# Performance work log

Hardware: AMD Instinct MI355X
Metric: run time of the kernel (lower is better)

## Reference

```python
import jax, jax.numpy as jnp
import numpy as np

B, S = 32, 4096
HID, MEM, ATT = 512, 512, 512


def setup_inputs() -> dict:
    key = jax.random.key(0)
    k1, k2, k3, k4, k5, k6, k7 = jax.random.split(key, 7)
    scale_h = 1.0 / np.sqrt(HID)
    scale_m = 1.0 / np.sqrt(MEM)
    scale_a = 1.0 / np.sqrt(ATT)
    return {
        "hidden": jax.random.normal(k1, (B, HID), dtype=jnp.float32),
        "memory": jax.random.normal(k2, (B, S, MEM), dtype=jnp.float32),
        "mem_pad": jnp.zeros((B, S), dtype=jnp.bool_),
        "coverage": jax.random.uniform(k3, (B, S), dtype=jnp.float32),
        # params stored as (in, out) so x @ W == torch Linear(x)
        "W_h": jax.random.uniform(k4, (HID, ATT), minval=-scale_h, maxval=scale_h, dtype=jnp.float32),
        "W_m": jax.random.uniform(k5, (MEM, ATT), minval=-scale_m, maxval=scale_m, dtype=jnp.float32),
        "W_c": jax.random.uniform(k6, (ATT,), minval=-1.0, maxval=1.0, dtype=jnp.float32),
        "v": jax.random.uniform(k7, (ATT,), minval=-scale_a, maxval=scale_a, dtype=jnp.float32),
    }


def reference(hidden, memory, mem_pad, coverage, W_h, W_m, W_c, v):
    h = hidden @ W_h                                   # (B, A)
    m = jnp.einsum('bsd,da->bsa', memory, W_m)         # (B, S, A)
    c_feat = coverage[..., None] * W_c                 # (B, S, A) ; Linear(1->A) == scalar * weight row
    score = jnp.einsum('bsa,a->bs', jnp.tanh(h[:, None, :] + m + c_feat), v)  # (B, S)
    score = jnp.where(mem_pad, -jnp.inf, score)
    attn_weights = jax.nn.softmax(score, axis=-1)      # (B, S)
    context = jnp.einsum('bs,bsd->bd', attn_weights, memory)  # (B, D)
    return context, attn_weights
```

## Files before the change

kernel.cpp:

```cpp
#include <hip/hip_runtime.h>
#include <hip/hip_bf16.h>
#include <math.h>

#define BB 32
#define SS 4096
#define DMEM 512
#define DATT 512

typedef short short8 __attribute__((ext_vector_type(8)));
typedef float floatx4 __attribute__((ext_vector_type(4)));

__device__ inline short f2bf(float x) {
    unsigned u = __float_as_uint(x);
    unsigned r = (u + 0x7fffu + ((u >> 16) & 1u)) >> 16;
    return (short)(r & 0xffffu);
}

__device__ inline float fast_tanh(float x) {
    float e = __expf(2.0f * x);
    float r = __builtin_amdgcn_rcpf(e + 1.0f);
    return __builtin_fmaf(-2.0f, r, 1.0f);
}

__device__ inline void gld_lds16(const void* g, void* l) {
    __builtin_amdgcn_global_load_lds(
        (const __attribute__((address_space(1))) unsigned int*)g,
        (__attribute__((address_space(3))) unsigned int*)l, 16, 0, 0);
}


__global__ void prep_wt_kernel(const float* __restrict__ Wm, short* __restrict__ Wt) {
    const int n0 = blockIdx.x * 32;
    const int k0 = blockIdx.y * 32;
    const int t = threadIdx.x;
    const int r = t >> 5, c = t & 31;
    __shared__ float lds[32 * 33];
#pragma unroll
    for (int j = 0; j < 4; ++j) {
        int kk = r + j * 8;
        lds[kk * 33 + c] = Wm[(size_t)(k0 + kk) * 512 + n0 + c];
    }
    __syncthreads();
#pragma unroll
    for (int j = 0; j < 4; ++j) {
        int nn = r + j * 8;
        Wt[(size_t)(n0 + nn) * 512 + k0 + c] = f2bf(lds[c * 33 + nn]);
    }
}

__global__ void prep_h_kernel(const float* __restrict__ hidden, const float* __restrict__ Wh,
                              float* __restrict__ h) {
    const int b = blockIdx.x;
    const int n = blockIdx.y * 256 + threadIdx.x;
    const int kc = blockIdx.z;
    float acc = 0.f;
#pragma unroll 8
    for (int k = kc * 128; k < kc * 128 + 128; ++k)
        acc += hidden[b * 512 + k] * Wh[(size_t)k * 512 + n];
    atomicAdd(&h[b * 512 + n], acc);
}


__global__ __launch_bounds__(512, 2)
void fused_kernel(const float* __restrict__ memory,
                  const float* __restrict__ coverage,
                  const unsigned char* __restrict__ pad,
                  const short* __restrict__ Wt,
                  const float* __restrict__ h,
                  const float* __restrict__ Wc,
                  const float* __restrict__ v,
                  float* __restrict__ pOut,
                  float* __restrict__ mWS,
                  float* __restrict__ lWS,
                  float* __restrict__ ctxPart) {
    const int blk = blockIdx.x;
    const int b = blk >> 5;
    const int st = blk & 31;
    const int s0 = st * 128;

    const int tid = threadIdx.x;
    const int lane = tid & 63;
    const int wave = tid >> 6;
    const int wm = wave & 1;
    const int wn = wave >> 1;
    const int col = lane & 15;
    const int q = lane >> 4;

    __shared__ __align__(16) char smem[77824];
    char* tileB0 = smem;
    char* tileB1 = smem + 32768;
    char* tileA  = smem + 65536;
    float* covS   = (float*)(smem + 73728);
    float* sred   = (float*)(smem + 74240);
    float* scoreS = (float*)(smem + 76288);
    float* pS     = (float*)(smem + 76800);
    float* mlS    = (float*)(smem + 77312);
    float4* red4  = (float4*)smem;

    if (tid < 128) covS[tid] = coverage[(size_t)b * SS + s0 + tid];

    const float4* gA4 = (const float4*)(memory + ((size_t)b * SS + s0) * 512);
    const char* gB = (const char*)Wt;

    float4 apf[2];

    floatx4 acc[4][8];
#pragma unroll
    for (int mi = 0; mi < 4; ++mi)
#pragma unroll
        for (int ni = 0; ni < 8; ++ni)
            acc[mi][ni] = (floatx4){0.f, 0.f, 0.f, 0.f};

#pragma unroll
    for (int j = 0; j < 2; ++j) {
        int s = j * 512 + tid;
        apf[j] = gA4[(size_t)(s >> 3) * 128 + (s & 7)];
    }
#pragma unroll
    for (int it = 0; it < 4; ++it) {
        int ci = it * 512 + tid;
        int row = ci >> 2;
        int gch = (ci & 3) ^ ((row >> 1) & 3);
        gld_lds16(gB + (size_t)row * 1024 + gch * 16,
                  tileB0 + it * 8192 + wave * 1024);
    }
#pragma unroll
    for (int j = 0; j < 2; ++j) {
        int s = j * 512 + tid;
        int row = s >> 3, l8 = s & 7;
        union { __hip_bfloat162 h2; unsigned u; } p0, p1;
        p0.h2 = __float22bfloat162_rn(make_float2(apf[j].x, apf[j].y));
        p1.h2 = __float22bfloat162_rn(make_float2(apf[j].z, apf[j].w));
        uint2 w; w.x = p0.u; w.y = p1.u;
        int off = row * 64 + (((l8 >> 1) ^ ((row >> 1) & 3)) << 4) + ((l8 & 1) << 3);
        *(uint2*)(tileA + off) = w;
    }
    __syncthreads();

    for (int kt = 0; kt < 16; ++kt) {
        if (kt < 15) {
#pragma unroll
            for (int j = 0; j < 2; ++j) {
                int s = j * 512 + tid;
                apf[j] = gA4[(size_t)(s >> 3) * 128 + (kt + 1) * 8 + (s & 7)];
            }
            char* ldsB = ((kt + 1) & 1) ? tileB1 : tileB0;
#pragma unroll
            for (int it = 0; it < 4; ++it) {
                int ci = it * 512 + tid;
                int row = ci >> 2;
                int gch = (ci & 3) ^ ((row >> 1) & 3);
                gld_lds16(gB + (size_t)row * 1024 + (kt + 1) * 64 + gch * 16,
                          ldsB + it * 8192 + wave * 1024);
            }
        }

        const char* bbase = (kt & 1) ? tileB1 : tileB0;
        short8 af[4], bf[8];
#pragma unroll
        for (int mi = 0; mi < 4; ++mi) {
            int row = wm * 64 + mi * 16 + col;
            af[mi] = *(const short8*)(tileA + row * 64 + ((q ^ ((row >> 1) & 3)) << 4));
        }
#pragma unroll
        for (int ni = 0; ni < 8; ++ni) {
            int row = wn * 128 + ni * 16 + col;
            bf[ni] = *(const short8*)(bbase + row * 64 + ((q ^ ((row >> 1) & 3)) << 4));
        }
#pragma unroll
        for (int mi = 0; mi < 4; ++mi)
#pragma unroll
            for (int ni = 0; ni < 8; ++ni)
                acc[mi][ni] = __builtin_amdgcn_mfma_f32_16x16x32_bf16(af[mi], bf[ni], acc[mi][ni], 0, 0, 0);

        __syncthreads();

        if (kt < 15) {
#pragma unroll
            for (int j = 0; j < 2; ++j) {
                int s = j * 512 + tid;
                int row = s >> 3, l8 = s & 7;
                union { __hip_bfloat162 h2; unsigned u; } p0, p1;
                p0.h2 = __float22bfloat162_rn(make_float2(apf[j].x, apf[j].y));
                p1.h2 = __float22bfloat162_rn(make_float2(apf[j].z, apf[j].w));
                uint2 w; w.x = p0.u; w.y = p1.u;
                int off = row * 64 + (((l8 >> 1) ^ ((row >> 1) & 3)) << 4) + ((l8 & 1) << 3);
                *(uint2*)(tileA + off) = w;
            }
            __syncthreads();
        }
    }

    float hv[8], wcv[8], vv[8];
#pragma unroll
    for (int ni = 0; ni < 8; ++ni) {
        int n = wn * 128 + ni * 16 + col;
        hv[ni] = h[b * 512 + n];
        wcv[ni] = Wc[n];
        vv[ni] = v[n];
    }
    float rowAcc[4][4];
#pragma unroll
    for (int mi = 0; mi < 4; ++mi)
#pragma unroll
        for (int r = 0; r < 4; ++r)
            rowAcc[mi][r] = 0.f;
#pragma unroll
    for (int mi = 0; mi < 4; ++mi) {
#pragma unroll
        for (int r = 0; r < 4; ++r) {
            float cv = covS[wm * 64 + mi * 16 + q * 4 + r];
#pragma unroll
            for (int ni = 0; ni < 8; ++ni) {
                float val = acc[mi][ni][r] + hv[ni] + cv * wcv[ni];
                rowAcc[mi][r] += fast_tanh(val) * vv[ni];
            }
        }
    }
#pragma unroll
    for (int off = 1; off < 16; off <<= 1)
#pragma unroll
        for (int mi = 0; mi < 4; ++mi)
#pragma unroll
            for (int r = 0; r < 4; ++r)
                rowAcc[mi][r] += __shfl_xor(rowAcc[mi][r], off, 64);

    if (col == 0) {
#pragma unroll
        for (int mi = 0; mi < 4; ++mi)
#pragma unroll
            for (int r = 0; r < 4; ++r)
                sred[wn * 128 + wm * 64 + mi * 16 + q * 4 + r] = rowAcc[mi][r];
    }
    __syncthreads();

    if (tid < 128) {
        float sc = sred[tid] + sred[128 + tid] + sred[256 + tid] + sred[384 + tid];
        if (pad[(size_t)b * SS + s0 + tid]) sc = -INFINITY;
        scoreS[tid] = sc;
    }
    __syncthreads();
    if (tid < 64) {
        float mx = fmaxf(scoreS[tid], scoreS[tid + 64]);
#pragma unroll
        for (int off = 32; off >= 1; off >>= 1) mx = fmaxf(mx, __shfl_xor(mx, off, 64));
        if (tid == 0) mlS[0] = mx;
    }
    __syncthreads();
    const float mtile = mlS[0];
    if (tid < 128) pS[tid] = __expf(scoreS[tid] - mtile);
    __syncthreads();
    if (tid < 64) {
        float sm = pS[tid] + pS[tid + 64];
#pragma unroll
        for (int off = 32; off >= 1; off >>= 1) sm += __shfl_xor(sm, off, 64);
        if (tid == 0) mlS[1] = sm;
    }
    __syncthreads();

    if (tid < 128) pOut[(size_t)b * SS + s0 + tid] = pS[tid];
    if (tid == 0) {
        mWS[b * 32 + st] = mtile;
        lWS[b * 32 + st] = mlS[1];
    }

    const int sg = tid >> 7;
    const int dc = tid & 127;
    const float4* m4 = (const float4*)(memory + ((size_t)b * SS + s0) * 512);
    float4 a4 = {0.f, 0.f, 0.f, 0.f};
#pragma unroll 8
    for (int i = 0; i < 32; ++i) {
        int s = sg * 32 + i;
        float w = pS[s];
        float4 f = m4[(size_t)s * 128 + dc];
        a4.x += w * f.x; a4.y += w * f.y; a4.z += w * f.z; a4.w += w * f.w;
    }
    red4[sg * 128 + dc] = a4;
    __syncthreads();
    if (tid < 128) {
        float4 r0 = red4[tid], r1 = red4[128 + tid], r2 = red4[256 + tid], r3 = red4[384 + tid];
        float4 o;
        o.x = r0.x + r1.x + r2.x + r3.x;
        o.y = r0.y + r1.y + r2.y + r3.y;
        o.z = r0.z + r1.z + r2.z + r3.z;
        o.w = r0.w + r1.w + r2.w + r3.w;
        ((float4*)(ctxPart + ((size_t)(b * 32 + st)) * 512))[tid] = o;
    }
}

__global__ __launch_bounds__(512)
void combine_kernel(const float* __restrict__ mWS,
                    const float* __restrict__ lWS,
                    const float* __restrict__ ctxPart,
                    float* __restrict__ ctx,
                    float* __restrict__ attn) {
    const int b = blockIdx.x;
    const int tid = threadIdx.x;
    __shared__ float scaleS[32];
    __shared__ float gS[2];

    if (tid < 64) {
        float mv = (tid < 32) ? mWS[b * 32 + tid] : -INFINITY;
#pragma unroll
        for (int off = 32; off >= 1; off >>= 1) mv = fmaxf(mv, __shfl_xor(mv, off, 64));
        if (tid == 0) gS[0] = mv;
    }
    __syncthreads();
    const float gmax = gS[0];
    if (tid < 64) {
        float sc = 0.f, lv = 0.f;
        if (tid < 32) {
            sc = __expf(mWS[b * 32 + tid] - gmax);
            scaleS[tid] = sc;
            lv = lWS[b * 32 + tid] * sc;
        }
#pragma unroll
        for (int off = 32; off >= 1; off >>= 1) lv += __shfl_xor(lv, off, 64);
        if (tid == 0) gS[1] = lv;
    }
    __syncthreads();
    const float inv = 1.0f / gS[1];

    float facc = 0.f;
#pragma unroll 8
    for (int st = 0; st < 32; ++st)
        facc += ctxPart[((size_t)(b * 32 + st)) * 512 + tid] * scaleS[st];
    ctx[b * 512 + tid] = facc * inv;

#pragma unroll
    for (int j = 0; j < 8; ++j) {
        size_t idx = (size_t)b * SS + j * 512 + tid;
        attn[idx] = attn[idx] * scaleS[(j * 512 + tid) >> 7] * inv;
    }
}

extern "C" void kernel_launch(void* const* d_in, const int* in_sizes, int n_in,
                              void* d_out, int out_size, void* d_ws, size_t ws_size,
                              hipStream_t stream) {
    (void)in_sizes; (void)n_in; (void)out_size; (void)ws_size;
    const float* hidden   = (const float*)d_in[0];
    const float* memory   = (const float*)d_in[1];
    const unsigned char* mem_pad = (const unsigned char*)d_in[2];
    const float* coverage = (const float*)d_in[3];
    const float* Wh       = (const float*)d_in[4];
    const float* Wm       = (const float*)d_in[5];
    const float* Wc       = (const float*)d_in[6];
    const float* v        = (const float*)d_in[7];

    char* ws = (char*)d_ws;
    short* Wt      = (short*)ws;
    float* h       = (float*)(ws + 512 * 1024);
    float* mWS     = (float*)(ws + 576 * 1024);
    float* lWS     = (float*)(ws + 580 * 1024);
    float* ctxPart = (float*)(ws + 584 * 1024);

    float* ctx  = (float*)d_out;
    float* attn = (float*)d_out + BB * 512;

    hipMemsetAsync(h, 0, BB * 512 * sizeof(float), stream);
    prep_wt_kernel<<<dim3(16, 16), dim3(256), 0, stream>>>(Wm, Wt);
    prep_h_kernel<<<dim3(32, 2, 4), dim3(256), 0, stream>>>(hidden, Wh, h);
    fused_kernel<<<dim3(BB * 32), dim3(512), 0, stream>>>(
        memory, coverage, mem_pad, Wt, h, Wc, v, attn, mWS, lWS, ctxPart);
    combine_kernel<<<dim3(BB), dim3(512), 0, stream>>>(mWS, lWS, ctxPart, ctx, attn);
}
```

Before: 481.5 us.

## Double block size to 1024 threads, halving per-wave GEMM tile width

```diff
diff --git a/kernel.cpp b/kernel.cpp
--- a/kernel.cpp
+++ b/kernel.cpp
@@ -61,7 +61,7 @@
 }
 
 
-__global__ __launch_bounds__(512, 2)
+__global__ __launch_bounds__(1024, 4)
 void fused_kernel(const float* __restrict__ memory,
                   const float* __restrict__ coverage,
                   const unsigned char* __restrict__ pad,
@@ -86,15 +86,15 @@
     const int col = lane & 15;
     const int q = lane >> 4;
 
-    __shared__ __align__(16) char smem[77824];
+    __shared__ __align__(16) char smem[79368];
     char* tileB0 = smem;
     char* tileB1 = smem + 32768;
     char* tileA  = smem + 65536;
     float* covS   = (float*)(smem + 73728);
     float* sred   = (float*)(smem + 74240);
-    float* scoreS = (float*)(smem + 76288);
-    float* pS     = (float*)(smem + 76800);
-    float* mlS    = (float*)(smem + 77312);
+    float* scoreS = (float*)(smem + 78336);
+    float* pS     = (float*)(smem + 78848);
+    float* mlS    = (float*)(smem + 79360);
     float4* red4  = (float4*)smem;
 
     if (tid < 128) covS[tid] = coverage[(size_t)b * SS + s0 + tid];
@@ -102,99 +102,83 @@
     const float4* gA4 = (const float4*)(memory + ((size_t)b * SS + s0) * 512);
     const char* gB = (const char*)Wt;
 
-    float4 apf[2];
-
-    floatx4 acc[4][8];
+    const int arow = tid >> 3, al8 = tid & 7;
+    const int aoff = arow * 64 + (((al8 >> 1) ^ ((arow >> 1) & 3)) << 4) + ((al8 & 1) << 3);
+    float4 apf;
+
+    floatx4 acc[4][4];
 #pragma unroll
     for (int mi = 0; mi < 4; ++mi)
 #pragma unroll
-        for (int ni = 0; ni < 8; ++ni)
+        for (int ni = 0; ni < 4; ++ni)
             acc[mi][ni] = (floatx4){0.f, 0.f, 0.f, 0.f};
 
-#pragma unroll
-    for (int j = 0; j < 2; ++j) {
-        int s = j * 512 + tid;
-        apf[j] = gA4[(size_t)(s >> 3) * 128 + (s & 7)];
-    }
-#pragma unroll
-    for (int it = 0; it < 4; ++it) {
-        int ci = it * 512 + tid;
+    apf = gA4[(size_t)arow * 128 + al8];
+#pragma unroll
+    for (int it = 0; it < 2; ++it) {
+        int ci = it * 1024 + tid;
         int row = ci >> 2;
         int gch = (ci & 3) ^ ((row >> 1) & 3);
         gld_lds16(gB + (size_t)row * 1024 + gch * 16,
-                  tileB0 + it * 8192 + wave * 1024);
-    }
-#pragma unroll
-    for (int j = 0; j < 2; ++j) {
-        int s = j * 512 + tid;
-        int row = s >> 3, l8 = s & 7;
+                  tileB0 + it * 16384 + wave * 1024);
+    }
+    {
         union { __hip_bfloat162 h2; unsigned u; } p0, p1;
-        p0.h2 = __float22bfloat162_rn(make_float2(apf[j].x, apf[j].y));
-        p1.h2 = __float22bfloat162_rn(make_float2(apf[j].z, apf[j].w));
+        p0.h2 = __float22bfloat162_rn(make_float2(apf.x, apf.y));
+        p1.h2 = __float22bfloat162_rn(make_float2(apf.z, apf.w));
         uint2 w; w.x = p0.u; w.y = p1.u;
-        int off = row * 64 + (((l8 >> 1) ^ ((row >> 1) & 3)) << 4) + ((l8 & 1) << 3);
-        *(uint2*)(tileA + off) = w;
+        *(uint2*)(tileA + aoff) = w;
     }
     __syncthreads();
 
     for (int kt = 0; kt < 16; ++kt) {
         if (kt < 15) {
-#pragma unroll
-            for (int j = 0; j < 2; ++j) {
-                int s = j * 512 + tid;
-                apf[j] = gA4[(size_t)(s >> 3) * 128 + (kt + 1) * 8 + (s & 7)];
-            }
+            apf = gA4[(size_t)arow * 128 + (kt + 1) * 8 + al8];
             char* ldsB = ((kt + 1) & 1) ? tileB1 : tileB0;
 #pragma unroll
-            for (int it = 0; it < 4; ++it) {
-                int ci = it * 512 + tid;
+            for (int it = 0; it < 2; ++it) {
+                int ci = it * 1024 + tid;
                 int row = ci >> 2;
                 int gch = (ci & 3) ^ ((row >> 1) & 3);
                 gld_lds16(gB + (size_t)row * 1024 + (kt + 1) * 64 + gch * 16,
-                          ldsB + it * 8192 + wave * 1024);
+                          ldsB + it * 16384 + wave * 1024);
             }
         }
 
         const char* bbase = (kt & 1) ? tileB1 : tileB0;
-        short8 af[4], bf[8];
+        short8 af[4], bf[4];
 #pragma unroll
         for (int mi = 0; mi < 4; ++mi) {
             int row = wm * 64 + mi * 16 + col;
             af[mi] = *(const short8*)(tileA + row * 64 + ((q ^ ((row >> 1) & 3)) << 4));
         }
 #pragma unroll
-        for (int ni = 0; ni < 8; ++ni) {
-            int row = wn * 128 + ni * 16 + col;
+        for (int ni = 0; ni < 4; ++ni) {
+            int row = wn * 64 + ni * 16 + col;
             bf[ni] = *(const short8*)(bbase + row * 64 + ((q ^ ((row >> 1) & 3)) << 4));
         }
 #pragma unroll
         for (int mi = 0; mi < 4; ++mi)
 #pragma unroll
-            for (int ni = 0; ni < 8; ++ni)
+            for (int ni = 0; ni < 4; ++ni)
                 acc[mi][ni] = __builtin_amdgcn_mfma_f32_16x16x32_bf16(af[mi], bf[ni], acc[mi][ni], 0, 0, 0);
 
         __syncthreads();
 
         if (kt < 15) {
-#pragma unroll
-            for (int j = 0; j < 2; ++j) {
-                int s = j * 512 + tid;
-                int row = s >> 3, l8 = s & 7;
-                union { __hip_bfloat162 h2; unsigned u; } p0, p1;
-                p0.h2 = __float22bfloat162_rn(make_float2(apf[j].x, apf[j].y));
-                p1.h2 = __float22bfloat162_rn(make_float2(apf[j].z, apf[j].w));
-                uint2 w; w.x = p0.u; w.y = p1.u;
-                int off = row * 64 + (((l8 >> 1) ^ ((row >> 1) & 3)) << 4) + ((l8 & 1) << 3);
-                *(uint2*)(tileA + off) = w;
-            }
+            union { __hip_bfloat162 h2; unsigned u; } p0, p1;
+            p0.h2 = __float22bfloat162_rn(make_float2(apf.x, apf.y));
+            p1.h2 = __float22bfloat162_rn(make_float2(apf.z, apf.w));
+            uint2 w; w.x = p0.u; w.y = p1.u;
+            *(uint2*)(tileA + aoff) = w;
             __syncthreads();
         }
     }
 
-    float hv[8], wcv[8], vv[8];
-#pragma unroll
-    for (int ni = 0; ni < 8; ++ni) {
-        int n = wn * 128 + ni * 16 + col;
+    float hv[4], wcv[4], vv[4];
+#pragma unroll
+    for (int ni = 0; ni < 4; ++ni) {
+        int n = wn * 64 + ni * 16 + col;
         hv[ni] = h[b * 512 + n];
         wcv[ni] = Wc[n];
         vv[ni] = v[n];
@@ -211,7 +195,7 @@
         for (int r = 0; r < 4; ++r) {
             float cv = covS[wm * 64 + mi * 16 + q * 4 + r];
 #pragma unroll
-            for (int ni = 0; ni < 8; ++ni) {
+            for (int ni = 0; ni < 4; ++ni) {
                 float val = acc[mi][ni][r] + hv[ni] + cv * wcv[ni];
                 rowAcc[mi][r] += fast_tanh(val) * vv[ni];
             }
@@ -235,7 +219,9 @@
     __syncthreads();
 
     if (tid < 128) {
-        float sc = sred[tid] + sred[128 + tid] + sred[256 + tid] + sred[384 + tid];
+        float sc = 0.f;
+#pragma unroll
+        for (int w = 0; w < 8; ++w) sc += sred[w * 128 + tid];
         if (pad[(size_t)b * SS + s0 + tid]) sc = -INFINITY;
         scoreS[tid] = sc;
     }
@@ -269,8 +255,8 @@
     const float4* m4 = (const float4*)(memory + ((size_t)b * SS + s0) * 512);
     float4 a4 = {0.f, 0.f, 0.f, 0.f};
 #pragma unroll 8
-    for (int i = 0; i < 32; ++i) {
-        int s = sg * 32 + i;
+    for (int i = 0; i < 16; ++i) {
+        int s = sg * 16 + i;
         float w = pS[s];
         float4 f = m4[(size_t)s * 128 + dc];
         a4.x += w * f.x; a4.y += w * f.y; a4.z += w * f.z; a4.w += w * f.w;
@@ -278,12 +264,12 @@
     red4[sg * 128 + dc] = a4;
     __syncthreads();
     if (tid < 128) {
-        float4 r0 = red4[tid], r1 = red4[128 + tid], r2 = red4[256 + tid], r3 = red4[384 + tid];
-        float4 o;
-        o.x = r0.x + r1.x + r2.x + r3.x;
-        o.y = r0.y + r1.y + r2.y + r3.y;
-        o.z = r0.z + r1.z + r2.z + r3.z;
-        o.w = r0.w + r1.w + r2.w + r3.w;
+        float4 o = {0.f, 0.f, 0.f, 0.f};
+#pragma unroll
+        for (int g2 = 0; g2 < 8; ++g2) {
+            float4 r = red4[g2 * 128 + tid];
+            o.x += r.x; o.y += r.y; o.z += r.z; o.w += r.w;
+        }
         ((float4*)(ctxPart + ((size_t)(b * 32 + st)) * 512))[tid] = o;
     }
 }
@@ -360,7 +346,7 @@
     hipMemsetAsync(h, 0, BB * 512 * sizeof(float), stream);
     prep_wt_kernel<<<dim3(16, 16), dim3(256), 0, stream>>>(Wm, Wt);
     prep_h_kernel<<<dim3(32, 2, 4), dim3(256), 0, stream>>>(hidden, Wh, h);
-    fused_kernel<<<dim3(BB * 32), dim3(512), 0, stream>>>(
+    fused_kernel<<<dim3(BB * 32), dim3(1024), 0, stream>>>(
         memory, coverage, mem_pad, Wt, h, Wc, v, attn, mWS, lWS, ctxPart);
     combine_kernel<<<dim3(BB), dim3(512), 0, stream>>>(mWS, lWS, ctxPart, ctx, attn);
 }
```

Result: no change. 489.6 us (+1.7%).
